# Optimization experiments

Hardware: AMD Instinct MI355X
Metric: run time of the kernel (lower is better)

## Reference

```python
import jax, jax.numpy as jnp
import numpy as np

N = 50000
E = 800000
IN = 128
H = 128
R = 8
OUT = 2
BN_EPS = 1e-5


def setup_inputs() -> dict:
    key = jax.random.key(0)
    ks = jax.random.split(key, 16)
    s1 = 1.0 / np.sqrt(IN)
    s2 = 1.0 / np.sqrt(H)
    return {
        "x": jax.random.normal(ks[0], (N, IN), dtype=jnp.float32),
        "edge_index": jax.random.randint(ks[1], (2, E), 0, N, dtype=jnp.int32),
        "edge_type": jax.random.randint(ks[2], (E,), 0, R, dtype=jnp.int32),
        # layer 1 RGCNConv params
        "w1": jax.random.normal(ks[3], (R, IN, H), dtype=jnp.float32) * s1,
        "root1": jax.random.normal(ks[4], (IN, H), dtype=jnp.float32) * s1,
        "b1": jnp.zeros((H,), dtype=jnp.float32),
        "g1": jnp.ones((H,), dtype=jnp.float32),
        "be1": jnp.zeros((H,), dtype=jnp.float32),
        # layer 2 RGCNConv params
        "w2": jax.random.normal(ks[5], (R, H, H), dtype=jnp.float32) * s2,
        "root2": jax.random.normal(ks[6], (H, H), dtype=jnp.float32) * s2,
        "b2": jnp.zeros((H,), dtype=jnp.float32),
        "g2": jnp.ones((H,), dtype=jnp.float32),
        "be2": jnp.zeros((H,), dtype=jnp.float32),
        # classifier
        "cw": jax.random.normal(ks[7], (H, OUT), dtype=jnp.float32) * s2,
        "cb": jnp.zeros((OUT,), dtype=jnp.float32),
    }


def rgcn_conv(x, src, tgt, et, W, root, b):
    """PyG-style RGCNConv with per-relation mean aggregation.

    out[v] = sum_r mean_{e: tgt=v, type=r} (x[src_e] @ W[r]) + x[v] @ root + b
    """
    n = x.shape[0]
    # per-(node, relation) in-degree for mean normalization
    comp = tgt * R + et  # composite segment id, [E]
    deg = jax.ops.segment_sum(jnp.ones_like(et, dtype=x.dtype), comp,
                              num_segments=n * R)
    inv_deg = jnp.where(deg > 0, 1.0 / jnp.maximum(deg, 1.0), 0.0)
    # transform every node by every relation weight: [n, R, out]
    xw = jnp.einsum('ni,rio->nro', x, W)
    # gather per-edge message and apply mean normalization: [E, out]
    msg = xw[src, et] * inv_deg[comp][:, None]
    agg = jax.ops.segment_sum(msg, tgt, num_segments=n)
    return agg + x @ root + b


def batchnorm(x, gamma, beta):
    # training-mode BatchNorm1d over node dim (biased variance, eps=1e-5)
    mean = jnp.mean(x, axis=0)
    var = jnp.mean(jnp.square(x - mean), axis=0)
    return gamma * (x - mean) * jax.lax.rsqrt(var + BN_EPS) + beta


def reference(x, edge_index, edge_type, w1, root1, b1, g1, be1,
              w2, root2, b2, g2, be2, cw, cb):
    src, tgt = edge_index[0], edge_index[1]
    h = rgcn_conv(x, src, tgt, edge_type, w1, root1, b1)
    h = jax.nn.relu(batchnorm(h, g1, be1))
    h = rgcn_conv(h, src, tgt, edge_type, w2, root2, b2)
    h = jax.nn.relu(batchnorm(h, g2, be2))
    return h @ cw + cb
```

## Files before the change

### kernel.cpp

```cpp
#include <hip/hip_runtime.h>
#include <hip/hip_bf16.h>

#define N_NODES 50000
#define N_EDGES 800000
#define DIM 128
#define NREL 8
#define KTOT 1152
#define NRSEG (N_NODES * NREL)
#define BN_EPS 1e-5f

typedef __attribute__((ext_vector_type(8))) short bf16x8;
typedef __attribute__((ext_vector_type(16))) float f32x16;

__device__ inline short f2b(float f) {
    __hip_bfloat16 h = __float2bfloat16(f);
    return *reinterpret_cast<short*>(&h);
}
__device__ inline void acc4(float4& s, const float4& v) {
    s.x += v.x; s.y += v.y; s.z += v.z; s.w += v.w;
}


__global__ void k_hist(const int* __restrict__ ei, const int* __restrict__ et,
                       int* __restrict__ cnt) {
    int e = blockIdx.x * 256 + threadIdx.x;
    if (e < N_EDGES) {
        int tgt = ei[N_EDGES + e];
        int r = et[e];
        atomicAdd(&cnt[tgt * NREL + r], 1);
    }
}

__global__ void k_alloc(const int* __restrict__ cnt, int* __restrict__ offs,
                        int* __restrict__ cursor) {
    int i = blockIdx.x * 256 + threadIdx.x;
    int lane = threadIdx.x & 63;
    int c = (i < NRSEG) ? cnt[i] : 0;
    int incl = c;
    #pragma unroll
    for (int d = 1; d < 64; d <<= 1) {
        int t = __shfl_up(incl, d, 64);
        if (lane >= d) incl += t;
    }
    int total = __shfl(incl, 63, 64);
    int base = 0;
    if (lane == 63) base = atomicAdd(cursor, total);
    base = __shfl(base, 63, 64);
    if (i < NRSEG) offs[i] = base + incl - c;
}

__global__ void k_fill(const int* __restrict__ ei, const int* __restrict__ et,
                       const int* __restrict__ offs, int* __restrict__ fillcur,
                       int* __restrict__ sorted) {
    int e = blockIdx.x * 256 + threadIdx.x;
    if (e < N_EDGES) {
        int src = ei[e];
        int tgt = ei[N_EDGES + e];
        int comp = tgt * NREL + et[e];
        int pos = atomicAdd(&fillcur[comp], 1);
        sorted[offs[comp] + pos] = src;
    }
}

__global__ void k_wconv2(const float* __restrict__ W1, const float* __restrict__ root1,
                         __hip_bfloat16* __restrict__ Bt1,
                         const float* __restrict__ W2, const float* __restrict__ root2,
                         __hip_bfloat16* __restrict__ Bt2) {
    int gidx = blockIdx.x * 256 + threadIdx.x;
    int which = gidx >= DIM * KTOT;
    int idx = which ? gidx - DIM * KTOT : gidx;
    const float* W = which ? W2 : W1;
    const float* root = which ? root2 : root1;
    __hip_bfloat16* Bt = which ? Bt2 : Bt1;
    int o = idx / KTOT, k = idx % KTOT;
    float v;
    if (k < NREL * DIM) {
        int r = k >> 7, i = k & 127;
        v = W[(r * DIM + i) * DIM + o];
    } else {
        int i = k - NREL * DIM;
        v = root[i * DIM + o];
    }
    Bt[idx] = __float2bfloat16(v);
}

__global__ __launch_bounds__(256) void k_buildA3(
        const float* __restrict__ xr,
        const int* __restrict__ cnt, const int* __restrict__ offs,
        const int* __restrict__ sorted,
        __hip_bfloat16* __restrict__ A) {
    int tid = threadIdx.x;
    int unit = tid >> 5, il = tid & 31;
    int node = blockIdx.x * 8 + unit;
    if (node >= N_NODES) return;
    int ch = il * 4;
    int c = 0, o = 0;
    if (il < 8) {
        c = cnt[node * NREL + il];
        o = offs[node * NREL + il];
    }
    int ubase = (tid & 63) & 32;
    int c8[8], o8[8];
    #pragma unroll
    for (int r = 0; r < 8; ++r) {
        c8[r] = __shfl(c, ubase + r, 64);
        o8[r] = __shfl(o, ubase + r, 64);
    }
    const float* xch = xr + ch;
    __hip_bfloat16* arow = A + (size_t)node * KTOT + ch;

    #pragma unroll
    for (int rp = 0; rp < 4; ++rp) {
        int ca = c8[2 * rp], oa = o8[2 * rp];
        int cb = c8[2 * rp + 1], ob = o8[2 * rp + 1];
        float4 s0 = {0.f, 0.f, 0.f, 0.f}, s1 = {0.f, 0.f, 0.f, 0.f};
        int mx = max(ca, cb);
        for (int i = 0; i < mx; i += 2) {
            int ia0 = (i < ca) ? sorted[oa + i] : -1;
            int ia1 = (i + 1 < ca) ? sorted[oa + i + 1] : -1;
            int ib0 = (i < cb) ? sorted[ob + i] : -1;
            int ib1 = (i + 1 < cb) ? sorted[ob + i + 1] : -1;
            float4 va0 = {0,0,0,0}, va1 = {0,0,0,0}, vb0 = {0,0,0,0}, vb1 = {0,0,0,0};
            if (ia0 >= 0) va0 = *(const float4*)(xch + (size_t)ia0 * DIM);
            if (ia1 >= 0) va1 = *(const float4*)(xch + (size_t)ia1 * DIM);
            if (ib0 >= 0) vb0 = *(const float4*)(xch + (size_t)ib0 * DIM);
            if (ib1 >= 0) vb1 = *(const float4*)(xch + (size_t)ib1 * DIM);
            acc4(s0, va0); acc4(s0, va1);
            acc4(s1, vb0); acc4(s1, vb1);
        }
        float inva = (ca > 0) ? 1.f / (float)ca : 0.f;
        float invb = (cb > 0) ? 1.f / (float)cb : 0.f;
        short4 outa, outb;
        outa.x = f2b(s0.x * inva); outa.y = f2b(s0.y * inva);
        outa.z = f2b(s0.z * inva); outa.w = f2b(s0.w * inva);
        outb.x = f2b(s1.x * invb); outb.y = f2b(s1.y * invb);
        outb.z = f2b(s1.z * invb); outb.w = f2b(s1.w * invb);
        *(short4*)(arow + (2 * rp) * DIM) = outa;
        *(short4*)(arow + (2 * rp + 1) * DIM) = outb;
    }
    float4 sv = *(const float4*)(xch + (size_t)node * DIM);
    short4 so;
    so.x = f2b(sv.x); so.y = f2b(sv.y); so.z = f2b(sv.z); so.w = f2b(sv.w);
    *(short4*)(arow + NREL * DIM) = so;
}

#define G3LOAD(kc, aB, bB)                                                    \
    {                                                                         \
        _Pragma("unroll")                                                     \
        for (int s = 0; s < 2; ++s) {                                         \
            int ko = ((kc) + s) * 16;                                         \
            aB[s] = *(const bf16x8*)(aBase + ko);                             \
            bB[s][0] = *(const bf16x8*)(bBase0 + ko);                         \
            bB[s][1] = *(const bf16x8*)(bBase1 + ko);                         \
        }                                                                     \
    }

#define G3MFMA(aB, bB)                                                        \
    {                                                                         \
        _Pragma("unroll")                                                     \
        for (int s = 0; s < 2; ++s) {                                         \
            acc0 = __builtin_amdgcn_mfma_f32_32x32x16_bf16(aB[s], bB[s][0], acc0, 0, 0, 0); \
            acc1 = __builtin_amdgcn_mfma_f32_32x32x16_bf16(aB[s], bB[s][1], acc1, 0, 0, 0); \
        }                                                                     \
    }

__global__ __launch_bounds__(64) void k_gemm3(const __hip_bfloat16* __restrict__ A,
                                              const __hip_bfloat16* __restrict__ Bt,
                                              const float* __restrict__ bias,
                                              float* __restrict__ h,
                                              float* __restrict__ stats) {
    int lane = threadIdx.x;
    int rt = blockIdx.x >> 1, ct = blockIdx.x & 1;
    int m0 = rt * 32, c0 = ct * 64;
    int half = lane >> 5, l31 = lane & 31;
    int arow = m0 + l31;
    if (arow >= N_NODES) arow = N_NODES - 1;
    const __hip_bfloat16* aBase = A + (size_t)arow * KTOT + half * 8;
    const __hip_bfloat16* bBase0 = Bt + (size_t)(c0 + l31) * KTOT + half * 8;
    const __hip_bfloat16* bBase1 = Bt + (size_t)(c0 + 32 + l31) * KTOT + half * 8;

    f32x16 acc0 = {}, acc1 = {};
    bf16x8 aA[2], aB2[2];
    bf16x8 bA[2][2], bB2[2][2];

    G3LOAD(0, aA, bA);
    for (int c = 0; c < 72; c += 4) {
        G3LOAD(c + 2, aB2, bB2);
        G3MFMA(aA, bA);
        if (c + 4 < 72) G3LOAD(c + 4, aA, bA);
        G3MFMA(aB2, bB2);
    }

    int col0 = c0 + l31, col1 = c0 + 32 + l31;
    float bv0 = bias[col0], bv1 = bias[col1];
    float s1a = 0.f, s2a = 0.f, s1b = 0.f, s2b = 0.f;
    #pragma unroll
    for (int reg = 0; reg < 16; ++reg) {
        int row = m0 + (reg & 3) + 8 * (reg >> 2) + 4 * half;
        if (row < N_NODES) {
            float v0 = acc0[reg] + bv0;
            float v1 = acc1[reg] + bv1;
            h[(size_t)row * DIM + col0] = v0;
            h[(size_t)row * DIM + col1] = v1;
            s1a += v0; s2a += v0 * v0;
            s1b += v1; s2b += v1 * v1;
        }
    }
    s1a += __shfl_xor(s1a, 32, 64); s2a += __shfl_xor(s2a, 32, 64);
    s1b += __shfl_xor(s1b, 32, 64); s2b += __shfl_xor(s2b, 32, 64);
    if (half == 0) {
        atomicAdd(&stats[col0], s1a);
        atomicAdd(&stats[128 + col0], s2a);
        atomicAdd(&stats[col1], s1b);
        atomicAdd(&stats[128 + col1], s2b);
    }
}

__global__ void k_castbn(const float* __restrict__ h, const float* __restrict__ stats,
                         const float* __restrict__ g, const float* __restrict__ be,
                         float* __restrict__ xr) {
    int i = (blockIdx.x * 256 + threadIdx.x) * 4;
    if (i >= N_NODES * DIM) return;
    int ch = i & 127;
    float4 v = *(const float4*)&h[i];
    float4 sm = *(const float4*)&stats[ch];
    float4 sq = *(const float4*)&stats[128 + ch];
    float4 gg = *(const float4*)&g[ch];
    float4 bb = *(const float4*)&be[ch];
    const float invn = 1.f / (float)N_NODES;
    float m, var, a, b;
    float4 o;
    m = sm.x * invn; var = sq.x * invn - m * m; a = gg.x * rsqrtf(var + BN_EPS); b = bb.x - m * a;
    o.x = fmaxf(v.x * a + b, 0.f);
    m = sm.y * invn; var = sq.y * invn - m * m; a = gg.y * rsqrtf(var + BN_EPS); b = bb.y - m * a;
    o.y = fmaxf(v.y * a + b, 0.f);
    m = sm.z * invn; var = sq.z * invn - m * m; a = gg.z * rsqrtf(var + BN_EPS); b = bb.z - m * a;
    o.z = fmaxf(v.z * a + b, 0.f);
    m = sm.w * invn; var = sq.w * invn - m * m; a = gg.w * rsqrtf(var + BN_EPS); b = bb.w - m * a;
    o.w = fmaxf(v.w * a + b, 0.f);
    *(float4*)&xr[i] = o;
}

__global__ void k_classifier(const float* __restrict__ h, const float* __restrict__ stats,
                             const float* __restrict__ g, const float* __restrict__ be,
                             const float* __restrict__ cw, const float* __restrict__ cb,
                             float* __restrict__ out) {
    int w = blockIdx.x * 4 + (threadIdx.x >> 6);
    int lane = threadIdx.x & 63;
    if (w >= N_NODES) return;
    int c = lane * 2;
    const float invn = 1.f / (float)N_NODES;
    float2 v = *(const float2*)&h[(size_t)w * DIM + c];
    float2 sm = *(const float2*)&stats[c];
    float2 sq = *(const float2*)&stats[128 + c];
    float2 gg = *(const float2*)&g[c];
    float2 bb = *(const float2*)&be[c];
    float m0 = sm.x * invn, var0 = sq.x * invn - m0 * m0;
    float a0 = gg.x * rsqrtf(var0 + BN_EPS), b0 = bb.x - m0 * a0;
    float m1 = sm.y * invn, var1 = sq.y * invn - m1 * m1;
    float a1 = gg.y * rsqrtf(var1 + BN_EPS), b1 = bb.y - m1 * a1;
    float p0 = fmaxf(v.x * a0 + b0, 0.f);
    float p1 = fmaxf(v.y * a1 + b1, 0.f);
    float acc0 = p0 * cw[c * 2] + p1 * cw[(c + 1) * 2];
    float acc1 = p0 * cw[c * 2 + 1] + p1 * cw[(c + 1) * 2 + 1];
    #pragma unroll
    for (int d = 32; d; d >>= 1) {
        acc0 += __shfl_down(acc0, d, 64);
        acc1 += __shfl_down(acc1, d, 64);
    }
    if (lane == 0) {
        out[w * 2] = acc0 + cb[0];
        out[w * 2 + 1] = acc1 + cb[1];
    }
}

extern "C" void kernel_launch(void* const* d_in, const int* in_sizes, int n_in,
                              void* d_out, int out_size, void* d_ws, size_t ws_size,
                              hipStream_t stream) {
    const float* x    = (const float*)d_in[0];
    const int*   ei   = (const int*)d_in[1];
    const int*   et   = (const int*)d_in[2];
    const float* w1   = (const float*)d_in[3];
    const float* root1= (const float*)d_in[4];
    const float* b1   = (const float*)d_in[5];
    const float* g1   = (const float*)d_in[6];
    const float* be1  = (const float*)d_in[7];
    const float* w2   = (const float*)d_in[8];
    const float* root2= (const float*)d_in[9];
    const float* b2   = (const float*)d_in[10];
    const float* g2   = (const float*)d_in[11];
    const float* be2  = (const float*)d_in[12];
    const float* cw   = (const float*)d_in[13];
    const float* cb   = (const float*)d_in[14];
    float* out = (float*)d_out;

    char* ws = (char*)d_ws;
    size_t off = 0;
    auto alloc = [&](size_t bytes) -> char* {
        char* p = ws + off;
        off += (bytes + 255) & ~(size_t)255;
        return p;
    };
    int*   cnt     = (int*)alloc((size_t)NRSEG * 4);
    int*   fillcur = (int*)alloc((size_t)NRSEG * 4);
    int*   cursor  = (int*)alloc(256);
    float* stats1  = (float*)alloc(1024);
    float* stats2  = (float*)alloc(1024);
    size_t zero_bytes = off;
    int*   offs    = (int*)alloc((size_t)NRSEG * 4);
    __hip_bfloat16* Bt1 = (__hip_bfloat16*)alloc((size_t)DIM * KTOT * 2);
    __hip_bfloat16* Bt2 = (__hip_bfloat16*)alloc((size_t)DIM * KTOT * 2);
    int*   sorted  = (int*)alloc((size_t)N_EDGES * 4);
    float* h1      = (float*)alloc((size_t)N_NODES * DIM * 4);
    float* h2      = (float*)alloc((size_t)N_NODES * DIM * 4);
    float* xr      = (float*)alloc((size_t)N_NODES * DIM * 4);
    __hip_bfloat16* A = (__hip_bfloat16*)alloc((size_t)N_NODES * KTOT * 2);

    hipMemsetAsync(d_ws, 0, zero_bytes, stream);

    k_hist<<<(N_EDGES + 255) / 256, 256, 0, stream>>>(ei, et, cnt);
    k_alloc<<<(NRSEG + 255) / 256, 256, 0, stream>>>(cnt, offs, cursor);
    k_fill<<<(N_EDGES + 255) / 256, 256, 0, stream>>>(ei, et, offs, fillcur, sorted);
    k_wconv2<<<2 * DIM * KTOT / 256, 256, 0, stream>>>(w1, root1, Bt1, w2, root2, Bt2);

    int bA_grid = (N_NODES + 7) / 8;
    int gemm_grid = ((N_NODES + 31) / 32) * 2;

    k_buildA3<<<bA_grid, 256, 0, stream>>>(x, cnt, offs, sorted, A);
    k_gemm3<<<gemm_grid, 64, 0, stream>>>(A, Bt1, b1, h1, stats1);

    k_castbn<<<(N_NODES * DIM / 4 + 255) / 256, 256, 0, stream>>>(h1, stats1, g1, be1, xr);
    k_buildA3<<<bA_grid, 256, 0, stream>>>(xr, cnt, offs, sorted, A);
    k_gemm3<<<gemm_grid, 64, 0, stream>>>(A, Bt2, b2, h2, stats2);

    k_classifier<<<(N_NODES + 3) / 4, 256, 0, stream>>>(h2, stats2, g2, be2, cw, cb, out);
}
```

Before: 620.9 us.

## Replace per-wave GEMM with LDS-tiled split-K GEMM plus finalize kernel

Swaps the 64-thread 32x64 register-only GEMM for a 256-thread 128x128 tile GEMM that double-buffers A and B tiles in shared memory, with K split in two across blocks writing fp32 partials. A new finalize kernel sums the two partials, adds bias, stores h in bf16, and accumulates BN statistics through a block reduction and atomics. The castbn and classifier kernels now read bf16 h. This is meant to raise data reuse and MFMA utilisation, at the cost of extra partial-buffer traffic, an added kernel launch, and bf16 rounding of h before BatchNorm.

After: 641.1 us. 1.03x slower.

```diff
diff --git a/kernel.cpp b/kernel.cpp
--- a/kernel.cpp
+++ b/kernel.cpp
@@ -8,10 +8,17 @@
 #define KTOT 1152
 #define NRSEG (N_NODES * NREL)
 #define BN_EPS 1e-5f
+#define KSPLIT 576
+#define LDSTRIDE 36
 
 typedef __attribute__((ext_vector_type(8))) short bf16x8;
 typedef __attribute__((ext_vector_type(16))) float f32x16;
 
+__device__ inline float b2f(short s) {
+    union { unsigned u; float f; } t;
+    t.u = ((unsigned)(unsigned short)s) << 16;
+    return t.f;
+}
 __device__ inline short f2b(float f) {
     __hip_bfloat16 h = __float2bfloat16(f);
     return *reinterpret_cast<short*>(&h);
@@ -144,104 +151,139 @@
     *(short4*)(arow + NREL * DIM) = so;
 }
 
-#define G3LOAD(kc, aB, bB)                                                    \
-    {                                                                         \
-        _Pragma("unroll")                                                     \
-        for (int s = 0; s < 2; ++s) {                                         \
-            int ko = ((kc) + s) * 16;                                         \
-            aB[s] = *(const bf16x8*)(aBase + ko);                             \
-            bB[s][0] = *(const bf16x8*)(bBase0 + ko);                         \
-            bB[s][1] = *(const bf16x8*)(bBase1 + ko);                         \
-        }                                                                     \
-    }
-
-#define G3MFMA(aB, bB)                                                        \
-    {                                                                         \
-        _Pragma("unroll")                                                     \
-        for (int s = 0; s < 2; ++s) {                                         \
-            acc0 = __builtin_amdgcn_mfma_f32_32x32x16_bf16(aB[s], bB[s][0], acc0, 0, 0, 0); \
-            acc1 = __builtin_amdgcn_mfma_f32_32x32x16_bf16(aB[s], bB[s][1], acc1, 0, 0, 0); \
-        }                                                                     \
-    }
-
-__global__ __launch_bounds__(64) void k_gemm3(const __hip_bfloat16* __restrict__ A,
-                                              const __hip_bfloat16* __restrict__ Bt,
-                                              const float* __restrict__ bias,
-                                              float* __restrict__ h,
-                                              float* __restrict__ stats) {
-    int lane = threadIdx.x;
-    int rt = blockIdx.x >> 1, ct = blockIdx.x & 1;
-    int m0 = rt * 32, c0 = ct * 64;
+__global__ __launch_bounds__(256) void k_gemm6(
+        const __hip_bfloat16* __restrict__ A,
+        const __hip_bfloat16* __restrict__ Bt,
+        float* __restrict__ p) {
+    __shared__ __hip_bfloat16 As[2][128 * LDSTRIDE];
+    __shared__ __hip_bfloat16 Bs[2][128 * LDSTRIDE];
+    int tid = threadIdx.x;
+    int rt = blockIdx.x >> 1, ks = blockIdx.x & 1;
+    int m0 = rt * 128;
+    int kbase = ks * KSPLIT;
+    float* pout = p + (size_t)ks * N_NODES * DIM;
+
+    int srow = tid >> 2, sslot = tid & 3;
+    int arow0 = m0 + srow;      if (arow0 >= N_NODES) arow0 = N_NODES - 1;
+    int arow1 = m0 + 64 + srow; if (arow1 >= N_NODES) arow1 = N_NODES - 1;
+    const __hip_bfloat16* aSrc0 = A + (size_t)arow0 * KTOT + kbase + sslot * 8;
+    const __hip_bfloat16* aSrc1 = A + (size_t)arow1 * KTOT + kbase + sslot * 8;
+    const __hip_bfloat16* bSrc0 = Bt + (size_t)srow * KTOT + kbase + sslot * 8;
+    const __hip_bfloat16* bSrc1 = Bt + (size_t)(64 + srow) * KTOT + kbase + sslot * 8;
+    int lds0 = srow * LDSTRIDE + sslot * 8;
+    int lds1 = (64 + srow) * LDSTRIDE + sslot * 8;
+
+    int lane = tid & 63, wid = tid >> 6;
+    int wr = wid >> 1, wc = wid & 1;
     int half = lane >> 5, l31 = lane & 31;
-    int arow = m0 + l31;
-    if (arow >= N_NODES) arow = N_NODES - 1;
-    const __hip_bfloat16* aBase = A + (size_t)arow * KTOT + half * 8;
-    const __hip_bfloat16* bBase0 = Bt + (size_t)(c0 + l31) * KTOT + half * 8;
-    const __hip_bfloat16* bBase1 = Bt + (size_t)(c0 + 32 + l31) * KTOT + half * 8;
-
-    f32x16 acc0 = {}, acc1 = {};
-    bf16x8 aA[2], aB2[2];
-    bf16x8 bA[2][2], bB2[2][2];
-
-    G3LOAD(0, aA, bA);
-    for (int c = 0; c < 72; c += 4) {
-        G3LOAD(c + 2, aB2, bB2);
-        G3MFMA(aA, bA);
-        if (c + 4 < 72) G3LOAD(c + 4, aA, bA);
-        G3MFMA(aB2, bB2);
-    }
-
-    int col0 = c0 + l31, col1 = c0 + 32 + l31;
-    float bv0 = bias[col0], bv1 = bias[col1];
-    float s1a = 0.f, s2a = 0.f, s1b = 0.f, s2b = 0.f;
-    #pragma unroll
-    for (int reg = 0; reg < 16; ++reg) {
-        int row = m0 + (reg & 3) + 8 * (reg >> 2) + 4 * half;
-        if (row < N_NODES) {
-            float v0 = acc0[reg] + bv0;
-            float v1 = acc1[reg] + bv1;
-            h[(size_t)row * DIM + col0] = v0;
-            h[(size_t)row * DIM + col1] = v1;
-            s1a += v0; s2a += v0 * v0;
-            s1b += v1; s2b += v1 * v1;
-        }
-    }
-    s1a += __shfl_xor(s1a, 32, 64); s2a += __shfl_xor(s2a, 32, 64);
-    s1b += __shfl_xor(s1b, 32, 64); s2b += __shfl_xor(s2b, 32, 64);
+    f32x16 acc00 = {}, acc01 = {}, acc10 = {}, acc11 = {};
+
+    bf16x8 la0 = *(const bf16x8*)aSrc0;
+    bf16x8 la1 = *(const bf16x8*)aSrc1;
+    bf16x8 lb0 = *(const bf16x8*)bSrc0;
+    bf16x8 lb1 = *(const bf16x8*)bSrc1;
+    *(bf16x8*)&As[0][lds0] = la0;
+    *(bf16x8*)&As[0][lds1] = la1;
+    *(bf16x8*)&Bs[0][lds0] = lb0;
+    *(bf16x8*)&Bs[0][lds1] = lb1;
+    __syncthreads();
+
+    #pragma unroll 1
+    for (int t = 0; t < KSPLIT / 32; ++t) {
+        int cur = t & 1;
+        if (t < KSPLIT / 32 - 1) {
+            int ko = (t + 1) * 32;
+            la0 = *(const bf16x8*)(aSrc0 + ko);
+            la1 = *(const bf16x8*)(aSrc1 + ko);
+            lb0 = *(const bf16x8*)(bSrc0 + ko);
+            lb1 = *(const bf16x8*)(bSrc1 + ko);
+        }
+        const __hip_bfloat16* as = As[cur];
+        const __hip_bfloat16* bs = Bs[cur];
+        #pragma unroll
+        for (int s = 0; s < 2; ++s) {
+            int slot = (s * 2 + half) * 8;
+            bf16x8 a0 = *(const bf16x8*)&as[(wr * 64 + l31) * LDSTRIDE + slot];
+            bf16x8 a1 = *(const bf16x8*)&as[(wr * 64 + 32 + l31) * LDSTRIDE + slot];
+            bf16x8 b0 = *(const bf16x8*)&bs[(wc * 64 + l31) * LDSTRIDE + slot];
+            bf16x8 b1 = *(const bf16x8*)&bs[(wc * 64 + 32 + l31) * LDSTRIDE + slot];
+            acc00 = __builtin_amdgcn_mfma_f32_32x32x16_bf16(a0, b0, acc00, 0, 0, 0);
+            acc01 = __builtin_amdgcn_mfma_f32_32x32x16_bf16(a0, b1, acc01, 0, 0, 0);
+            acc10 = __builtin_amdgcn_mfma_f32_32x32x16_bf16(a1, b0, acc10, 0, 0, 0);
+            acc11 = __builtin_amdgcn_mfma_f32_32x32x16_bf16(a1, b1, acc11, 0, 0, 0);
+        }
+        if (t < KSPLIT / 32 - 1) {
+            int nxt = cur ^ 1;
+            *(bf16x8*)&As[nxt][lds0] = la0;
+            *(bf16x8*)&As[nxt][lds1] = la1;
+            *(bf16x8*)&Bs[nxt][lds0] = lb0;
+            *(bf16x8*)&Bs[nxt][lds1] = lb1;
+        }
+        __syncthreads();
+    }
+
+    #pragma unroll
+    for (int m = 0; m < 2; ++m) {
+        const f32x16& am0 = m ? acc10 : acc00;
+        const f32x16& am1 = m ? acc11 : acc01;
+        #pragma unroll
+        for (int reg = 0; reg < 16; ++reg) {
+            int row = m0 + wr * 64 + m * 32 + (reg & 3) + 8 * (reg >> 2) + 4 * half;
+            if (row < N_NODES) {
+                pout[(size_t)row * DIM + wc * 64 + l31]      = am0[reg];
+                pout[(size_t)row * DIM + wc * 64 + 32 + l31] = am1[reg];
+            }
+        }
+    }
+}
+
+__global__ void k_fin(const float* __restrict__ p, const float* __restrict__ bias,
+                      __hip_bfloat16* __restrict__ h, float* __restrict__ stats) {
+    int c = threadIdx.x & 127;
+    int half = threadIdx.x >> 7;
+    const float* p1 = p + (size_t)N_NODES * DIM;
+    float bv = bias[c];
+    float s = 0.f, q = 0.f;
+    for (int v = blockIdx.x * 2 + half; v < N_NODES; v += gridDim.x * 2) {
+        size_t idx = (size_t)v * DIM + c;
+        float x = p[idx] + p1[idx] + bv;
+        h[idx] = __float2bfloat16(x);
+        s += x; q += x * x;
+    }
+    __shared__ float ls[256], lq[256];
+    ls[threadIdx.x] = s; lq[threadIdx.x] = q;
+    __syncthreads();
     if (half == 0) {
-        atomicAdd(&stats[col0], s1a);
-        atomicAdd(&stats[128 + col0], s2a);
-        atomicAdd(&stats[col1], s1b);
-        atomicAdd(&stats[128 + col1], s2b);
-    }
-}
-
-__global__ void k_castbn(const float* __restrict__ h, const float* __restrict__ stats,
+        s += ls[c + 128]; q += lq[c + 128];
+        atomicAdd(&stats[c], s);
+        atomicAdd(&stats[128 + c], q);
+    }
+}
+
+__global__ void k_castbn(const __hip_bfloat16* __restrict__ h, const float* __restrict__ stats,
                          const float* __restrict__ g, const float* __restrict__ be,
                          float* __restrict__ xr) {
-    int i = (blockIdx.x * 256 + threadIdx.x) * 4;
+    int i = (blockIdx.x * 256 + threadIdx.x) * 8;
     if (i >= N_NODES * DIM) return;
     int ch = i & 127;
-    float4 v = *(const float4*)&h[i];
-    float4 sm = *(const float4*)&stats[ch];
-    float4 sq = *(const float4*)&stats[128 + ch];
-    float4 gg = *(const float4*)&g[ch];
-    float4 bb = *(const float4*)&be[ch];
+    bf16x8 v = *(const bf16x8*)&h[i];
     const float invn = 1.f / (float)N_NODES;
-    float m, var, a, b;
-    float4 o;
-    m = sm.x * invn; var = sq.x * invn - m * m; a = gg.x * rsqrtf(var + BN_EPS); b = bb.x - m * a;
-    o.x = fmaxf(v.x * a + b, 0.f);
-    m = sm.y * invn; var = sq.y * invn - m * m; a = gg.y * rsqrtf(var + BN_EPS); b = bb.y - m * a;
-    o.y = fmaxf(v.y * a + b, 0.f);
-    m = sm.z * invn; var = sq.z * invn - m * m; a = gg.z * rsqrtf(var + BN_EPS); b = bb.z - m * a;
-    o.z = fmaxf(v.z * a + b, 0.f);
-    m = sm.w * invn; var = sq.w * invn - m * m; a = gg.w * rsqrtf(var + BN_EPS); b = bb.w - m * a;
-    o.w = fmaxf(v.w * a + b, 0.f);
-    *(float4*)&xr[i] = o;
-}
-
-__global__ void k_classifier(const float* __restrict__ h, const float* __restrict__ stats,
+    float o[8];
+    #pragma unroll
+    for (int j = 0; j < 8; ++j) {
+        float m = stats[ch + j] * invn;
+        float var = stats[128 + ch + j] * invn - m * m;
+        float a = g[ch + j] * rsqrtf(var + BN_EPS);
+        float b = be[ch + j] - m * a;
+        o[j] = fmaxf(b2f(v[j]) * a + b, 0.f);
+    }
+    float4 o0 = {o[0], o[1], o[2], o[3]};
+    float4 o1 = {o[4], o[5], o[6], o[7]};
+    *(float4*)&xr[i] = o0;
+    *(float4*)&xr[i + 4] = o1;
+}
+
+__global__ void k_classifier(const __hip_bfloat16* __restrict__ h, const float* __restrict__ stats,
                              const float* __restrict__ g, const float* __restrict__ be,
                              const float* __restrict__ cw, const float* __restrict__ cb,
                              float* __restrict__ out) {
@@ -250,17 +292,13 @@
     if (w >= N_NODES) return;
     int c = lane * 2;
     const float invn = 1.f / (float)N_NODES;
-    float2 v = *(const float2*)&h[(size_t)w * DIM + c];
-    float2 sm = *(const float2*)&stats[c];
-    float2 sq = *(const float2*)&stats[128 + c];
-    float2 gg = *(const float2*)&g[c];
-    float2 bb = *(const float2*)&be[c];
-    float m0 = sm.x * invn, var0 = sq.x * invn - m0 * m0;
-    float a0 = gg.x * rsqrtf(var0 + BN_EPS), b0 = bb.x - m0 * a0;
-    float m1 = sm.y * invn, var1 = sq.y * invn - m1 * m1;
-    float a1 = gg.y * rsqrtf(var1 + BN_EPS), b1 = bb.y - m1 * a1;
-    float p0 = fmaxf(v.x * a0 + b0, 0.f);
-    float p1 = fmaxf(v.y * a1 + b1, 0.f);
+    __hip_bfloat162 hv = *(const __hip_bfloat162*)&h[(size_t)w * DIM + c];
+    float m0 = stats[c] * invn, var0 = stats[128 + c] * invn - m0 * m0;
+    float a0 = g[c] * rsqrtf(var0 + BN_EPS), b0 = be[c] - m0 * a0;
+    float m1 = stats[c + 1] * invn, var1 = stats[128 + c + 1] * invn - m1 * m1;
+    float a1 = g[c + 1] * rsqrtf(var1 + BN_EPS), b1 = be[c + 1] - m1 * a1;
+    float p0 = fmaxf(__bfloat162float(hv.x) * a0 + b0, 0.f);
+    float p1 = fmaxf(__bfloat162float(hv.y) * a1 + b1, 0.f);
     float acc0 = p0 * cw[c * 2] + p1 * cw[(c + 1) * 2];
     float acc1 = p0 * cw[c * 2 + 1] + p1 * cw[(c + 1) * 2 + 1];
     #pragma unroll
@@ -311,10 +349,11 @@
     __hip_bfloat16* Bt1 = (__hip_bfloat16*)alloc((size_t)DIM * KTOT * 2);
     __hip_bfloat16* Bt2 = (__hip_bfloat16*)alloc((size_t)DIM * KTOT * 2);
     int*   sorted  = (int*)alloc((size_t)N_EDGES * 4);
-    float* h1      = (float*)alloc((size_t)N_NODES * DIM * 4);
-    float* h2      = (float*)alloc((size_t)N_NODES * DIM * 4);
-    float* xr      = (float*)alloc((size_t)N_NODES * DIM * 4);
-    __hip_bfloat16* A = (__hip_bfloat16*)alloc((size_t)N_NODES * KTOT * 2);
+    float* p       = (float*)alloc((size_t)2 * N_NODES * DIM * 4);
+    float* xr      = p;
+    __hip_bfloat16* h1 = (__hip_bfloat16*)alloc((size_t)N_NODES * DIM * 2);
+    __hip_bfloat16* h2 = (__hip_bfloat16*)alloc((size_t)N_NODES * DIM * 2);
+    __hip_bfloat16* A  = (__hip_bfloat16*)alloc((size_t)N_NODES * KTOT * 2);
 
     hipMemsetAsync(d_ws, 0, zero_bytes, stream);
 
@@ -324,14 +363,16 @@
     k_wconv2<<<2 * DIM * KTOT / 256, 256, 0, stream>>>(w1, root1, Bt1, w2, root2, Bt2);
 
     int bA_grid = (N_NODES + 7) / 8;
-    int gemm_grid = ((N_NODES + 31) / 32) * 2;
+    int gemm_grid = ((N_NODES + 127) / 128) * 2;
 
     k_buildA3<<<bA_grid, 256, 0, stream>>>(x, cnt, offs, sorted, A);
-    k_gemm3<<<gemm_grid, 64, 0, stream>>>(A, Bt1, b1, h1, stats1);
-
-    k_castbn<<<(N_NODES * DIM / 4 + 255) / 256, 256, 0, stream>>>(h1, stats1, g1, be1, xr);
+    k_gemm6<<<gemm_grid, 256, 0, stream>>>(A, Bt1, p);
+    k_fin<<<256, 256, 0, stream>>>(p, b1, h1, stats1);
+    k_castbn<<<(N_NODES * DIM / 8 + 255) / 256, 256, 0, stream>>>(h1, stats1, g1, be1, xr);
+
     k_buildA3<<<bA_grid, 256, 0, stream>>>(xr, cnt, offs, sorted, A);
-    k_gemm3<<<gemm_grid, 64, 0, stream>>>(A, Bt2, b2, h2, stats2);
+    k_gemm6<<<gemm_grid, 256, 0, stream>>>(A, Bt2, p);
+    k_fin<<<256, 256, 0, stream>>>(p, b2, h2, stats2);
 
     k_classifier<<<(N_NODES + 3) / 4, 256, 0, stream>>>(h2, stats2, g2, be2, cw, cb, out);
 }
```
